# Kernel optimization log

Hardware: AMD Instinct MI355X
Metric: run time of the kernel (lower is better)

The kernel has to match this reference:

```python
import jax, jax.numpy as jnp
import numpy as np

B, TQ, TK, D = 16, 1024, 4096, 512


def setup_inputs() -> dict:
    key = jax.random.key(0)
    k1, k2, k3 = jax.random.split(key, 3)
    decoder_output = jax.random.normal(k1, (B, TQ, D), dtype=jnp.float32)
    encoder_output = jax.random.normal(k2, (B, TK, D), dtype=jnp.float32)
    # Keras Dense(lstm_size): kernel [D, D] (glorot-ish scale), bias [D] (zeros init)
    W_a = jax.random.normal(k3, (D, D), dtype=jnp.float32) * (1.0 / np.sqrt(D))
    b_a = jnp.zeros((D,), dtype=jnp.float32)
    return {"decoder_output": decoder_output, "encoder_output": encoder_output,
            "W_a": W_a, "b_a": b_a}


def reference(decoder_output, encoder_output, W_a, b_a):
    # Luong 'general' attention:
    # proj = Dense(encoder_output)            [B, Tk, D]
    proj = jnp.einsum('bkd,de->bke', encoder_output, W_a) + b_a
    # score = dec @ proj^T                    [B, Tq, Tk]
    score = jnp.einsum('bqd,bkd->bqk', decoder_output, proj)
    # softmax over encoder time axis (tf axis=2 == last axis here)
    alignment_vector = jax.nn.softmax(score, axis=-1)
    # context = align @ encoder_output        [B, Tq, D]
    context_vector = jnp.einsum('bqk,bkd->bqd', alignment_vector, encoder_output)
    return (context_vector, alignment_vector)
```

## Files before the change

### kernel.cpp

```cpp
#include <hip/hip_runtime.h>
#include <hip/hip_bf16.h>

#define B_  16
#define TQ_ 1024
#define TK_ 4096
#define D_  512

typedef unsigned short u16;
typedef __attribute__((ext_vector_type(8))) short short8;
typedef __attribute__((ext_vector_type(8))) _Float16 f16x8;
typedef __attribute__((ext_vector_type(4))) float f32x4;

__device__ __forceinline__ u16 bf16_rne(float x) {
  unsigned u = __float_as_uint(x);
  u += 0x7FFFu + ((u >> 16) & 1u);
  return (u16)(u >> 16);
}
__device__ __forceinline__ float bf16_as_f32(u16 h) {
  return __uint_as_float(((unsigned)h) << 16);
}
__device__ __forceinline__ void split_bf16(float x, u16& h, u16& l) {
  u16 hh = bf16_rne(x);
  h = hh;
  l = bf16_rne(x - bf16_as_f32(hh));
}

__device__ __forceinline__ void glld16(const void* g, void* lds) {
  __builtin_amdgcn_global_load_lds(
      (const __attribute__((address_space(1))) unsigned int*)g,
      (__attribute__((address_space(3))) unsigned int*)lds, 16, 0, 0);
}

__global__ __launch_bounds__(256) void transpose_conv_kernel(
    const float* __restrict__ E, _Float16* __restrict__ ET)
{
  __shared__ float tile[64][65];
  const int b  = blockIdx.z;
  const int k0 = blockIdx.x * 64;
  const int d0 = blockIdx.y * 64;
  const float* Eb = E + (long long)b * TK_ * D_;
  _Float16* ETb = ET + (long long)b * D_ * TK_;

  const int t  = threadIdx.x;
  const int r  = t >> 2;
  const int c4 = (t & 3) * 16;

  #pragma unroll
  for (int i = 0; i < 16; i += 4) {
    float4 v = *(const float4*)&Eb[(long long)(k0 + r) * D_ + d0 + c4 + i];
    tile[r][c4 + i + 0] = v.x;
    tile[r][c4 + i + 1] = v.y;
    tile[r][c4 + i + 2] = v.z;
    tile[r][c4 + i + 3] = v.w;
  }
  __syncthreads();

  __align__(16) _Float16 h[16];
  #pragma unroll
  for (int i = 0; i < 16; ++i) h[i] = (_Float16)tile[c4 + i][r];
  uint4* dst = (uint4*)&ETb[(long long)(d0 + r) * TK_ + k0 + c4];
  dst[0] = ((const uint4*)h)[0];
  dst[1] = ((const uint4*)h)[1];
}

#define DBM 128
#define DBN 128
#define DBK 32
#define DPAD 40

__global__ __launch_bounds__(256) void gemm_dec2_kernel(
    const float* __restrict__ A, const float* __restrict__ Bm,
    _Float16* __restrict__ Ch, _Float16* __restrict__ Cl)
{
  __shared__ u16 Ah[DBM * DPAD];
  __shared__ u16 Al[DBM * DPAD];
  __shared__ u16 Bh[DBN * DPAD];
  __shared__ u16 Bl[DBN * DPAD];

  const float* Ab = A  + (long long)(blockIdx.y * DBM) * D_;
  const float* Bb = Bm + (long long)(blockIdx.x * DBN) * D_;

  const int t    = threadIdx.x;
  const int r    = t >> 1;
  const int hf   = t & 1;
  const int lane = t & 63;
  const int wave = t >> 6;
  const int wr   = (wave >> 1) * 64;
  const int wc   = (wave & 1) * 64;
  const int ln   = lane & 15;
  const int qd   = lane >> 4;

  f32x4 acc[4][4];
  #pragma unroll
  for (int i = 0; i < 4; ++i)
    #pragma unroll
    for (int j = 0; j < 4; ++j) { f32x4 z = {0.f,0.f,0.f,0.f}; acc[i][j] = z; }

  const float* srcA = Ab + (long long)r * D_ + hf * 16;
  const float* srcB = Bb + (long long)r * D_ + hf * 16;
  u16* dAh = &Ah[r * DPAD + hf * 16];
  u16* dAl = &Al[r * DPAD + hf * 16];
  u16* dBh = &Bh[r * DPAD + hf * 16];
  u16* dBl = &Bl[r * DPAD + hf * 16];

  for (int k0 = 0; k0 < D_; k0 += DBK) {
    {
      __align__(16) u16 h[16], l[16];
      #pragma unroll
      for (int i = 0; i < 16; i += 4) {
        float4 v = *(const float4*)(srcA + k0 + i);
        split_bf16(v.x, h[i+0], l[i+0]);
        split_bf16(v.y, h[i+1], l[i+1]);
        split_bf16(v.z, h[i+2], l[i+2]);
        split_bf16(v.w, h[i+3], l[i+3]);
      }
      ((uint4*)dAh)[0] = ((const uint4*)h)[0];
      ((uint4*)dAh)[1] = ((const uint4*)h)[1];
      ((uint4*)dAl)[0] = ((const uint4*)l)[0];
      ((uint4*)dAl)[1] = ((const uint4*)l)[1];
      #pragma unroll
      for (int i = 0; i < 16; i += 4) {
        float4 v = *(const float4*)(srcB + k0 + i);
        split_bf16(v.x, h[i+0], l[i+0]);
        split_bf16(v.y, h[i+1], l[i+1]);
        split_bf16(v.z, h[i+2], l[i+2]);
        split_bf16(v.w, h[i+3], l[i+3]);
      }
      ((uint4*)dBh)[0] = ((const uint4*)h)[0];
      ((uint4*)dBh)[1] = ((const uint4*)h)[1];
      ((uint4*)dBl)[0] = ((const uint4*)l)[0];
      ((uint4*)dBl)[1] = ((const uint4*)l)[1];
    }
    __syncthreads();

    short8 fah[4], fal[4], fbh[4], fbl[4];
    #pragma unroll
    for (int i = 0; i < 4; ++i) {
      int ra = (wr + i * 16 + ln) * DPAD + qd * 8;
      int rb = (wc + i * 16 + ln) * DPAD + qd * 8;
      fah[i] = *(const short8*)&Ah[ra];
      fal[i] = *(const short8*)&Al[ra];
      fbh[i] = *(const short8*)&Bh[rb];
      fbl[i] = *(const short8*)&Bl[rb];
    }
    #pragma unroll
    for (int i = 0; i < 4; ++i)
      #pragma unroll
      for (int j = 0; j < 4; ++j) {
        acc[i][j] = __builtin_amdgcn_mfma_f32_16x16x32_bf16(fah[i], fbh[j], acc[i][j], 0, 0, 0);
        acc[i][j] = __builtin_amdgcn_mfma_f32_16x16x32_bf16(fah[i], fbl[j], acc[i][j], 0, 0, 0);
        acc[i][j] = __builtin_amdgcn_mfma_f32_16x16x32_bf16(fal[i], fbh[j], acc[i][j], 0, 0, 0);
      }
    __syncthreads();
  }

  const int m0 = blockIdx.y * DBM;
  const int n0 = blockIdx.x * DBN;
  #pragma unroll
  for (int i = 0; i < 4; ++i)
    #pragma unroll
    for (int j = 0; j < 4; ++j)
      #pragma unroll
      for (int rg = 0; rg < 4; ++rg) {
        int row = m0 + wr + i * 16 + qd * 4 + rg;
        int col = n0 + wc + j * 16 + ln;
        float x = acc[i][j][rg];
        _Float16 h = (_Float16)x;
        _Float16 l = (_Float16)(x - (float)h);
        long long idx = (long long)row * D_ + col;
        Ch[idx] = h;
        Cl[idx] = l;
      }
}

#define SBM 128
#define SBN 128
#define SBK 32

__global__ __launch_bounds__(256) void gemm_score_kernel(
    const _Float16* __restrict__ A_h, const _Float16* __restrict__ A_l,
    const float* __restrict__ Bf, float* __restrict__ C)
{
  __shared__ _Float16 sAh[SBM * SBK];
  __shared__ _Float16 sAl[SBM * SBK];
  __shared__ _Float16 sB [SBN * SBK];

  const int bz = blockIdx.z;
  const int m0 = blockIdx.y * SBM;
  const int n0 = blockIdx.x * SBN;
  const _Float16* Ahb = A_h + (long long)bz * TQ_ * D_ + (long long)m0 * D_;
  const _Float16* Alb = A_l + (long long)bz * TQ_ * D_ + (long long)m0 * D_;
  const float*    Bb  = Bf  + (long long)bz * TK_ * D_ + (long long)n0 * D_;

  const int t    = threadIdx.x;
  const int lane = t & 63;
  const int wave = t >> 6;
  const int wr   = (wave >> 1) * 64;
  const int wc   = (wave & 1) * 64;
  const int ln   = lane & 15;
  const int qd   = lane >> 4;

  f32x4 acc[4][4];
  #pragma unroll
  for (int i = 0; i < 4; ++i)
    #pragma unroll
    for (int j = 0; j < 4; ++j) { f32x4 z = {0.f,0.f,0.f,0.f}; acc[i][j] = z; }

  const int c0   = wave * 2;
  const int arow = c0 * 16 + (lane >> 2);
  const int ab   = (lane & 3) * 16;
  const char* gAh = (const char*)Ahb + (long long)arow * D_ * 2 + ab;
  const char* gAl = (const char*)Alb + (long long)arow * D_ * 2 + ab;
  const long long rstep = (long long)16 * D_ * 2;
  char* lAh = (char*)sAh + c0 * 1024 + lane * 16;
  char* lAl = (char*)sAl + c0 * 1024 + lane * 16;

  const int brow = t >> 1;
  const int bhf  = t & 1;
  const float* srcB = Bb + (long long)brow * D_ + bhf * 16;
  _Float16* dB = &sB[brow * SBK + bhf * 16];

  for (int k0 = 0; k0 < D_; k0 += SBK) {
    glld16(gAh + (long long)k0 * 2, lAh);
    glld16(gAh + (long long)k0 * 2 + rstep, lAh + 1024);
    glld16(gAl + (long long)k0 * 2, lAl);
    glld16(gAl + (long long)k0 * 2 + rstep, lAl + 1024);
    {
      __align__(16) _Float16 hb[16];
      #pragma unroll
      for (int i = 0; i < 16; i += 4) {
        float4 v = *(const float4*)(srcB + k0 + i);
        hb[i+0] = (_Float16)v.x;
        hb[i+1] = (_Float16)v.y;
        hb[i+2] = (_Float16)v.z;
        hb[i+3] = (_Float16)v.w;
      }
      ((uint4*)dB)[0] = ((const uint4*)hb)[0];
      ((uint4*)dB)[1] = ((const uint4*)hb)[1];
    }
    __syncthreads();

    f16x8 fah[4], fal[4], fb[4];
    #pragma unroll
    for (int i = 0; i < 4; ++i) {
      int ra = (wr + i * 16 + ln) * SBK + qd * 8;
      int rb = (wc + i * 16 + ln) * SBK + qd * 8;
      fah[i] = *(const f16x8*)&sAh[ra];
      fal[i] = *(const f16x8*)&sAl[ra];
      fb[i]  = *(const f16x8*)&sB[rb];
    }
    #pragma unroll
    for (int i = 0; i < 4; ++i)
      #pragma unroll
      for (int j = 0; j < 4; ++j) {
        acc[i][j] = __builtin_amdgcn_mfma_f32_16x16x32_f16(fah[i], fb[j], acc[i][j], 0, 0, 0);
        acc[i][j] = __builtin_amdgcn_mfma_f32_16x16x32_f16(fal[i], fb[j], acc[i][j], 0, 0, 0);
      }
    __syncthreads();
  }

  float* Cb = C + (long long)bz * TQ_ * TK_;
  #pragma unroll
  for (int i = 0; i < 4; ++i)
    #pragma unroll
    for (int j = 0; j < 4; ++j)
      #pragma unroll
      for (int rg = 0; rg < 4; ++rg) {
        int row = m0 + wr + i * 16 + qd * 4 + rg;
        int col = n0 + wc + j * 16 + ln;
        Cb[(long long)row * TK_ + col] = acc[i][j][rg];
      }
}

__global__ __launch_bounds__(256) void softmax_kernel(float* __restrict__ P)
{
  __shared__ float red[8];
  float* p = P + (long long)blockIdx.x * TK_;
  const int t    = threadIdx.x;
  const int lane = t & 63;
  const int wave = t >> 6;

  float4 v[4];
  float mx = -3.0e38f;
  #pragma unroll
  for (int i = 0; i < 4; ++i) {
    v[i] = *(const float4*)&p[i * 1024 + t * 4];
    mx = fmaxf(mx, fmaxf(fmaxf(v[i].x, v[i].y), fmaxf(v[i].z, v[i].w)));
  }
  #pragma unroll
  for (int o = 32; o > 0; o >>= 1) mx = fmaxf(mx, __shfl_xor(mx, o, 64));
  if (lane == 0) red[wave] = mx;
  __syncthreads();
  mx = fmaxf(fmaxf(red[0], red[1]), fmaxf(red[2], red[3]));

  float s = 0.f;
  #pragma unroll
  for (int i = 0; i < 4; ++i) {
    v[i].x = __expf(v[i].x - mx);
    v[i].y = __expf(v[i].y - mx);
    v[i].z = __expf(v[i].z - mx);
    v[i].w = __expf(v[i].w - mx);
    s += (v[i].x + v[i].y) + (v[i].z + v[i].w);
  }
  #pragma unroll
  for (int o = 32; o > 0; o >>= 1) s += __shfl_xor(s, o, 64);
  if (lane == 0) red[4 + wave] = s;
  __syncthreads();
  s = (red[4] + red[5]) + (red[6] + red[7]);
  const float inv = 1.0f / s;

  #pragma unroll
  for (int i = 0; i < 4; ++i) {
    v[i].x *= inv; v[i].y *= inv; v[i].z *= inv; v[i].w *= inv;
    *(float4*)&p[i * 1024 + t * 4] = v[i];
  }
}

#define CBM 64
#define CBN 256
#define CBK 32

__global__ __launch_bounds__(512) void gemm_ctx_kernel(
    const float* __restrict__ P, const _Float16* __restrict__ ET,
    float* __restrict__ C)
{
  __shared__ _Float16 sA[CBM * CBK];
  __shared__ _Float16 sB[CBN * CBK];

  const int bz = blockIdx.z;
  const int m0 = blockIdx.y * CBM;
  const int n0 = blockIdx.x * CBN;
  const float*    Pb = P  + (long long)bz * TQ_ * TK_ + (long long)m0 * TK_;
  const _Float16* Eb = ET + (long long)bz * D_ * TK_  + (long long)n0 * TK_;

  const int t    = threadIdx.x;
  const int lane = t & 63;
  const int wave = t >> 6;
  const int wr   = (wave >> 2) * 32;
  const int wc   = (wave & 3) * 64;
  const int ln   = lane & 15;
  const int qd   = lane >> 4;

  f32x4 acc[2][4];
  #pragma unroll
  for (int i = 0; i < 2; ++i)
    #pragma unroll
    for (int j = 0; j < 4; ++j) { f32x4 z = {0.f,0.f,0.f,0.f}; acc[i][j] = z; }

  const int c0   = wave * 2;
  const int brow = c0 * 16 + (lane >> 2);
  const int bb   = (lane & 3) * 16;
  const char* gB = (const char*)Eb + (long long)brow * TK_ * 2 + bb;
  const long long rstep = (long long)16 * TK_ * 2;
  char* lB = (char*)sB + c0 * 1024 + lane * 16;

  const int arow = t >> 3;
  const int aseg = t & 7;
  const float* gA = Pb + (long long)arow * TK_ + aseg * 4;
  _Float16* lA = &sA[arow * CBK + aseg * 4];

  for (int k0 = 0; k0 < TK_; k0 += CBK) {
    glld16(gB + (long long)k0 * 2, lB);
    glld16(gB + (long long)k0 * 2 + rstep, lB + 1024);
    {
      float4 v = *(const float4*)(gA + k0);
      union { _Float16 h[4]; uint2 u; } pk;
      pk.h[0] = (_Float16)v.x;
      pk.h[1] = (_Float16)v.y;
      pk.h[2] = (_Float16)v.z;
      pk.h[3] = (_Float16)v.w;
      *(uint2*)lA = pk.u;
    }
    __syncthreads();

    f16x8 fa[2], fb[4];
    #pragma unroll
    for (int i = 0; i < 2; ++i)
      fa[i] = *(const f16x8*)&sA[(wr + i * 16 + ln) * CBK + qd * 8];
    #pragma unroll
    for (int j = 0; j < 4; ++j)
      fb[j] = *(const f16x8*)&sB[(wc + j * 16 + ln) * CBK + qd * 8];
    #pragma unroll
    for (int i = 0; i < 2; ++i)
      #pragma unroll
      for (int j = 0; j < 4; ++j)
        acc[i][j] = __builtin_amdgcn_mfma_f32_16x16x32_f16(fa[i], fb[j], acc[i][j], 0, 0, 0);
    __syncthreads();
  }

  float* Cb = C + (long long)bz * TQ_ * D_;
  #pragma unroll
  for (int i = 0; i < 2; ++i)
    #pragma unroll
    for (int j = 0; j < 4; ++j)
      #pragma unroll
      for (int rg = 0; rg < 4; ++rg) {
        int row = m0 + wr + i * 16 + qd * 4 + rg;
        int col = n0 + wc + j * 16 + ln;
        Cb[(long long)row * D_ + col] = acc[i][j][rg];
      }
}

extern "C" void kernel_launch(void* const* d_in, const int* in_sizes, int n_in,
                              void* d_out, int out_size, void* d_ws, size_t ws_size,
                              hipStream_t stream) {
  (void)in_sizes; (void)n_in; (void)out_size; (void)ws_size;
  const float* dec = (const float*)d_in[0];
  const float* enc = (const float*)d_in[1];
  const float* Wa  = (const float*)d_in[2];

  float* ctx   = (float*)d_out;
  float* align = ctx + (long long)B_ * TQ_ * D_;

  _Float16* dec2h = (_Float16*)d_ws;
  _Float16* dec2l = dec2h + (size_t)B_ * TQ_ * D_;
  _Float16* encT  = dec2l + (size_t)B_ * TQ_ * D_;

  transpose_conv_kernel<<<dim3(TK_ / 64, D_ / 64, B_), 256, 0, stream>>>(enc, encT);

  gemm_dec2_kernel<<<dim3(D_ / DBN, (B_ * TQ_) / DBM, 1), 256, 0, stream>>>(
      dec, Wa, dec2h, dec2l);

  gemm_score_kernel<<<dim3(TK_ / SBN, TQ_ / SBM, B_), 256, 0, stream>>>(
      dec2h, dec2l, enc, align);

  softmax_kernel<<<B_ * TQ_, 256, 0, stream>>>(align);

  gemm_ctx_kernel<<<dim3(D_ / CBN, TQ_ / CBM, B_), 512, 0, stream>>>(align, encT, ctx);
}
```

Baseline: 887.4 us.

## Precompute fp16 operands in workspace and XOR-swizzle LDS tiles in GEMMs

The transpose kernel now also writes an fp16 row-major copy of the encoder. When the workspace is large enough, the score GEMM loads that copy directly into LDS with async global-to-LDS loads instead of converting fp32 in registers. The softmax additionally writes an fp16 copy of the probabilities so the context GEMM can load A the same way. LDS layouts in both GEMMs are XOR-swizzled to cut bank conflicts. The cost is extra global writes, more workspace, and a dependence on ws_size deciding which path runs; the p16 buffer reuses the dec2 and encF workspace region after those buffers are no longer needed.

```diff
diff --git a/kernel.cpp b/kernel.cpp
--- a/kernel.cpp
+++ b/kernel.cpp
@@ -31,8 +31,13 @@
       (__attribute__((address_space(3))) unsigned int*)lds, 16, 0, 0);
 }
 
+__device__ __forceinline__ int seg_src(int l) {
+  return (l & 3) ^ ((l >> 2) & 3) ^ ((l >> 4) & 3);
+}
+
 __global__ __launch_bounds__(256) void transpose_conv_kernel(
-    const float* __restrict__ E, _Float16* __restrict__ ET)
+    const float* __restrict__ E, _Float16* __restrict__ ET,
+    _Float16* __restrict__ EF)
 {
   __shared__ float tile[64][65];
   const int b  = blockIdx.z;
@@ -45,6 +50,7 @@
   const int r  = t >> 2;
   const int c4 = (t & 3) * 16;
 
+  __align__(16) _Float16 g[16];
   #pragma unroll
   for (int i = 0; i < 16; i += 4) {
     float4 v = *(const float4*)&Eb[(long long)(k0 + r) * D_ + d0 + c4 + i];
@@ -52,6 +58,16 @@
     tile[r][c4 + i + 1] = v.y;
     tile[r][c4 + i + 2] = v.z;
     tile[r][c4 + i + 3] = v.w;
+    g[i + 0] = (_Float16)v.x;
+    g[i + 1] = (_Float16)v.y;
+    g[i + 2] = (_Float16)v.z;
+    g[i + 3] = (_Float16)v.w;
+  }
+  if (EF) {
+    _Float16* EFb = EF + (long long)b * TK_ * D_;
+    uint4* dstF = (uint4*)&EFb[(long long)(k0 + r) * D_ + d0 + c4];
+    dstF[0] = ((const uint4*)g)[0];
+    dstF[1] = ((const uint4*)g)[1];
   }
   __syncthreads();
 
@@ -177,9 +193,11 @@
 #define SBN 128
 #define SBK 32
 
+template<bool F16B>
 __global__ __launch_bounds__(256) void gemm_score_kernel(
     const _Float16* __restrict__ A_h, const _Float16* __restrict__ A_l,
-    const float* __restrict__ Bf, float* __restrict__ C)
+    const float* __restrict__ Bf, const _Float16* __restrict__ B16,
+    float* __restrict__ C)
 {
   __shared__ _Float16 sAh[SBM * SBK];
   __shared__ _Float16 sAl[SBM * SBK];
@@ -190,7 +208,6 @@
   const int n0 = blockIdx.x * SBN;
   const _Float16* Ahb = A_h + (long long)bz * TQ_ * D_ + (long long)m0 * D_;
   const _Float16* Alb = A_l + (long long)bz * TQ_ * D_ + (long long)m0 * D_;
-  const float*    Bb  = Bf  + (long long)bz * TK_ * D_ + (long long)n0 * D_;
 
   const int t    = threadIdx.x;
   const int lane = t & 63;
@@ -199,6 +216,7 @@
   const int wc   = (wave & 1) * 64;
   const int ln   = lane & 15;
   const int qd   = lane >> 4;
+  const int sw   = qd ^ (ln & 3) ^ (ln >> 2);
 
   f32x4 acc[4][4];
   #pragma unroll
@@ -208,24 +226,37 @@
 
   const int c0   = wave * 2;
   const int arow = c0 * 16 + (lane >> 2);
-  const int ab   = (lane & 3) * 16;
+  const int ab   = seg_src(lane) * 16;
   const char* gAh = (const char*)Ahb + (long long)arow * D_ * 2 + ab;
   const char* gAl = (const char*)Alb + (long long)arow * D_ * 2 + ab;
   const long long rstep = (long long)16 * D_ * 2;
   char* lAh = (char*)sAh + c0 * 1024 + lane * 16;
   char* lAl = (char*)sAl + c0 * 1024 + lane * 16;
-
+  char* lB  = (char*)sB  + c0 * 1024 + lane * 16;
+
+  const char* gB16 = nullptr;
+  if constexpr (F16B) {
+    const _Float16* Bb16 = B16 + (long long)bz * TK_ * D_ + (long long)n0 * D_;
+    gB16 = (const char*)Bb16 + (long long)arow * D_ * 2 + ab;
+  }
+
+  const float* Bb = Bf + (long long)bz * TK_ * D_ + (long long)n0 * D_;
   const int brow = t >> 1;
   const int bhf  = t & 1;
   const float* srcB = Bb + (long long)brow * D_ + bhf * 16;
-  _Float16* dB = &sB[brow * SBK + bhf * 16];
+  const int bh2 = (brow & 3) ^ ((brow >> 2) & 3);
+  _Float16* dB0 = &sB[brow * SBK + ((2 * bhf    ) ^ bh2) * 8];
+  _Float16* dB1 = &sB[brow * SBK + ((2 * bhf + 1) ^ bh2) * 8];
 
   for (int k0 = 0; k0 < D_; k0 += SBK) {
     glld16(gAh + (long long)k0 * 2, lAh);
     glld16(gAh + (long long)k0 * 2 + rstep, lAh + 1024);
     glld16(gAl + (long long)k0 * 2, lAl);
     glld16(gAl + (long long)k0 * 2 + rstep, lAl + 1024);
-    {
+    if constexpr (F16B) {
+      glld16(gB16 + (long long)k0 * 2, lB);
+      glld16(gB16 + (long long)k0 * 2 + rstep, lB + 1024);
+    } else {
       __align__(16) _Float16 hb[16];
       #pragma unroll
       for (int i = 0; i < 16; i += 4) {
@@ -235,16 +266,16 @@
         hb[i+2] = (_Float16)v.z;
         hb[i+3] = (_Float16)v.w;
       }
-      ((uint4*)dB)[0] = ((const uint4*)hb)[0];
-      ((uint4*)dB)[1] = ((const uint4*)hb)[1];
+      *(uint4*)dB0 = ((const uint4*)hb)[0];
+      *(uint4*)dB1 = ((const uint4*)hb)[1];
     }
     __syncthreads();
 
     f16x8 fah[4], fal[4], fb[4];
     #pragma unroll
     for (int i = 0; i < 4; ++i) {
-      int ra = (wr + i * 16 + ln) * SBK + qd * 8;
-      int rb = (wc + i * 16 + ln) * SBK + qd * 8;
+      int ra = (wr + i * 16 + ln) * SBK + sw * 8;
+      int rb = (wc + i * 16 + ln) * SBK + sw * 8;
       fah[i] = *(const f16x8*)&sAh[ra];
       fal[i] = *(const f16x8*)&sAl[ra];
       fb[i]  = *(const f16x8*)&sB[rb];
@@ -272,7 +303,9 @@
       }
 }
 
-__global__ __launch_bounds__(256) void softmax_kernel(float* __restrict__ P)
+template<bool WP16>
+__global__ __launch_bounds__(256) void softmax_kernel(
+    float* __restrict__ P, _Float16* __restrict__ P16)
 {
   __shared__ float red[8];
   float* p = P + (long long)blockIdx.x * TK_;
@@ -309,10 +342,19 @@
   s = (red[4] + red[5]) + (red[6] + red[7]);
   const float inv = 1.0f / s;
 
+  _Float16* p16 = WP16 ? (P16 + (long long)blockIdx.x * TK_) : nullptr;
   #pragma unroll
   for (int i = 0; i < 4; ++i) {
     v[i].x *= inv; v[i].y *= inv; v[i].z *= inv; v[i].w *= inv;
     *(float4*)&p[i * 1024 + t * 4] = v[i];
+    if constexpr (WP16) {
+      union { _Float16 h[4]; uint2 u; } pk;
+      pk.h[0] = (_Float16)v[i].x;
+      pk.h[1] = (_Float16)v[i].y;
+      pk.h[2] = (_Float16)v[i].z;
+      pk.h[3] = (_Float16)v[i].w;
+      *(uint2*)&p16[i * 1024 + t * 4] = pk.u;
+    }
   }
 }
 
@@ -320,9 +362,10 @@
 #define CBN 256
 #define CBK 32
 
+template<bool F16A>
 __global__ __launch_bounds__(512) void gemm_ctx_kernel(
-    const float* __restrict__ P, const _Float16* __restrict__ ET,
-    float* __restrict__ C)
+    const float* __restrict__ P, const _Float16* __restrict__ P16,
+    const _Float16* __restrict__ ET, float* __restrict__ C)
 {
   __shared__ _Float16 sA[CBM * CBK];
   __shared__ _Float16 sB[CBN * CBK];
@@ -340,6 +383,7 @@
   const int wc   = (wave & 3) * 64;
   const int ln   = lane & 15;
   const int qd   = lane >> 4;
+  const int sw   = qd ^ (ln & 3) ^ (ln >> 2);
 
   f32x4 acc[2][4];
   #pragma unroll
@@ -349,20 +393,31 @@
 
   const int c0   = wave * 2;
   const int brow = c0 * 16 + (lane >> 2);
-  const int bb   = (lane & 3) * 16;
+  const int bb   = seg_src(lane) * 16;
   const char* gB = (const char*)Eb + (long long)brow * TK_ * 2 + bb;
   const long long rstep = (long long)16 * TK_ * 2;
   char* lB = (char*)sB + c0 * 1024 + lane * 16;
 
+  const char* gA16 = nullptr;
+  char* lA16 = nullptr;
+  if constexpr (F16A) {
+    const _Float16* Pb16 = P16 + (long long)bz * TQ_ * TK_ + (long long)m0 * TK_;
+    const int acrow = wave * 16 + (lane >> 2);
+    gA16 = (const char*)Pb16 + (long long)acrow * TK_ * 2 + bb;
+    lA16 = (char*)sA + wave * 1024 + lane * 16;
+  }
   const int arow = t >> 3;
   const int aseg = t & 7;
   const float* gA = Pb + (long long)arow * TK_ + aseg * 4;
-  _Float16* lA = &sA[arow * CBK + aseg * 4];
+  const int ah2 = (arow & 3) ^ ((arow >> 2) & 3);
+  _Float16* lA = &sA[arow * CBK + (((aseg >> 1) ^ ah2) * 8) + (aseg & 1) * 4];
 
   for (int k0 = 0; k0 < TK_; k0 += CBK) {
     glld16(gB + (long long)k0 * 2, lB);
     glld16(gB + (long long)k0 * 2 + rstep, lB + 1024);
-    {
+    if constexpr (F16A) {
+      if (wave < 4) glld16(gA16 + (long long)k0 * 2, lA16);
+    } else {
       float4 v = *(const float4*)(gA + k0);
       union { _Float16 h[4]; uint2 u; } pk;
       pk.h[0] = (_Float16)v.x;
@@ -376,10 +431,10 @@
     f16x8 fa[2], fb[4];
     #pragma unroll
     for (int i = 0; i < 2; ++i)
-      fa[i] = *(const f16x8*)&sA[(wr + i * 16 + ln) * CBK + qd * 8];
+      fa[i] = *(const f16x8*)&sA[(wr + i * 16 + ln) * CBK + sw * 8];
     #pragma unroll
     for (int j = 0; j < 4; ++j)
-      fb[j] = *(const f16x8*)&sB[(wc + j * 16 + ln) * CBK + qd * 8];
+      fb[j] = *(const f16x8*)&sB[(wc + j * 16 + ln) * CBK + sw * 8];
     #pragma unroll
     for (int i = 0; i < 2; ++i)
       #pragma unroll
@@ -404,7 +459,7 @@
 extern "C" void kernel_launch(void* const* d_in, const int* in_sizes, int n_in,
                               void* d_out, int out_size, void* d_ws, size_t ws_size,
                               hipStream_t stream) {
-  (void)in_sizes; (void)n_in; (void)out_size; (void)ws_size;
+  (void)in_sizes; (void)n_in; (void)out_size;
   const float* dec = (const float*)d_in[0];
   const float* enc = (const float*)d_in[1];
   const float* Wa  = (const float*)d_in[2];
@@ -412,19 +467,43 @@
   float* ctx   = (float*)d_out;
   float* align = ctx + (long long)B_ * TQ_ * D_;
 
-  _Float16* dec2h = (_Float16*)d_ws;
-  _Float16* dec2l = dec2h + (size_t)B_ * TQ_ * D_;
-  _Float16* encT  = dec2l + (size_t)B_ * TQ_ * D_;
-
-  transpose_conv_kernel<<<dim3(TK_ / 64, D_ / 64, B_), 256, 0, stream>>>(enc, encT);
+  char* ws = (char*)d_ws;
+  const size_t SZ_ENCT = (size_t)B_ * D_ * TK_ * 2;
+  const size_t SZ_DEC2 = (size_t)B_ * TQ_ * D_ * 2;
+  const size_t SZ_ENCF = (size_t)B_ * TK_ * D_ * 2;
+  const size_t SZ_P16  = (size_t)B_ * TQ_ * TK_ * 2;
+
+  _Float16* encT  = (_Float16*)(ws);
+  _Float16* dec2h = (_Float16*)(ws + SZ_ENCT);
+  _Float16* dec2l = (_Float16*)(ws + SZ_ENCT + SZ_DEC2);
+  _Float16* encF  = (_Float16*)(ws + SZ_ENCT + 2 * SZ_DEC2);
+  _Float16* p16   = (_Float16*)(ws + SZ_ENCT);
+
+  const bool mid  = ws_size >= SZ_ENCT + 2 * SZ_DEC2 + SZ_ENCF;
+  const bool full = ws_size >= SZ_ENCT + SZ_P16;
+
+  transpose_conv_kernel<<<dim3(TK_ / 64, D_ / 64, B_), 256, 0, stream>>>(
+      enc, encT, mid ? encF : nullptr);
 
   gemm_dec2_kernel<<<dim3(D_ / DBN, (B_ * TQ_) / DBM, 1), 256, 0, stream>>>(
       dec, Wa, dec2h, dec2l);
 
-  gemm_score_kernel<<<dim3(TK_ / SBN, TQ_ / SBM, B_), 256, 0, stream>>>(
-      dec2h, dec2l, enc, align);
-
-  softmax_kernel<<<B_ * TQ_, 256, 0, stream>>>(align);
-
-  gemm_ctx_kernel<<<dim3(D_ / CBN, TQ_ / CBM, B_), 512, 0, stream>>>(align, encT, ctx);
-}
+  if (mid)
+    gemm_score_kernel<true><<<dim3(TK_ / SBN, TQ_ / SBM, B_), 256, 0, stream>>>(
+        dec2h, dec2l, enc, encF, align);
+  else
+    gemm_score_kernel<false><<<dim3(TK_ / SBN, TQ_ / SBM, B_), 256, 0, stream>>>(
+        dec2h, dec2l, enc, nullptr, align);
+
+  if (full)
+    softmax_kernel<true><<<B_ * TQ_, 256, 0, stream>>>(align, p16);
+  else
+    softmax_kernel<false><<<B_ * TQ_, 256, 0, stream>>>(align, nullptr);
+
+  if (full)
+    gemm_ctx_kernel<true><<<dim3(D_ / CBN, TQ_ / CBM, B_), 512, 0, stream>>>(
+        align, p16, encT, ctx);
+  else
+    gemm_ctx_kernel<false><<<dim3(D_ / CBN, TQ_ / CBM, B_), 512, 0, stream>>>(
+        align, nullptr, encT, ctx);
+}
```

After: 866.4 us. -2.4%, faster.
